# Performance work log

Measured on AMD Instinct MI355X. Metric: run time of the kernel, lower is better.

## Reference

```python
import jax, jax.numpy as jnp
import numpy as np
import math

B, T, D, H, K = 4, 2048, 1024, 16, 64

def setup_inputs() -> dict:
    key = jax.random.key(0)
    ks = jax.random.split(key, 6)
    scale = 1.0 / math.sqrt(D)  # keep logits in a sane range (torch code uses raw randn params)
    X = jax.random.normal(ks[0], (B, T, D), dtype=jnp.float32)
    Wq = jax.random.normal(ks[1], (H, D, K), dtype=jnp.float32) * scale
    Wk = jax.random.normal(ks[2], (H, D, K), dtype=jnp.float32) * scale
    Wv = jax.random.normal(ks[3], (H, D, K), dtype=jnp.float32) * scale
    Wo = jax.random.normal(ks[4], (H * K, H * K), dtype=jnp.float32) * (1.0 / math.sqrt(H * K))
    bo = jnp.zeros((H * K,), dtype=jnp.float32)
    return {"X": X, "Wq": Wq, "Wk": Wk, "Wv": Wv, "Wo": Wo, "bo": bo}

def reference(X, Wq, Wk, Wv, Wo, bo):
    # per-head projections: [B,H,T,K]
    q = jnp.einsum('btc,nck->bntk', X, Wq)
    k = jnp.einsum('btc,nck->bntk', X, Wk)
    v = jnp.einsum('btc,nck->bntk', X, Wv)
    # full score matrix [B,H,T,T] with causal mask (query t attends to s <= t)
    scores = jnp.einsum('bntk,bnsk->bnts', q, k) / math.sqrt(K)
    causal = jnp.tril(jnp.ones((T, T), dtype=bool))
    scores = jnp.where(causal[None, None], scores, jnp.finfo(scores.dtype).min)
    attn = jax.nn.softmax(scores, axis=-1)
    out = jnp.einsum('bnts,bnsk->bntk', attn, v)  # [B,H,T,K]
    # concat heads along feature dim (head-major ordering, matches torch.cat over heads)
    out = jnp.transpose(out, (0, 2, 1, 3)).reshape(B, T, H * K)
    # output projection (torch nn.Linear: x @ W.T + b)
    return out @ Wo.T + bo
```

## Files before the change

### kernel.cpp

```cpp
#include <hip/hip_runtime.h>
#include <hip/hip_bf16.h>
#include <math.h>

#define B_SZ 4
#define T_SZ 2048
#define D_SZ 1024
#define H_SZ 16
#define K_SZ 64

typedef __attribute__((ext_vector_type(8))) short bf8_t;
typedef __attribute__((ext_vector_type(4))) float f4_t;

__device__ __forceinline__ ushort f2bf(float f) {
    union { float f; unsigned u; } v; v.f = f;
    return (ushort)((v.u + 0x7fffu + ((v.u >> 16) & 1u)) >> 16);
}

__device__ __forceinline__ void gld_lds16(const ushort* g, ushort* l) {
    __builtin_amdgcn_global_load_lds(
        (const __attribute__((address_space(1))) void*)g,
        (__attribute__((address_space(3))) void*)l, 16, 0, 0);
}

__global__ __launch_bounds__(256) void convert_bf16_kernel(
    const float* __restrict__ src, ushort* __restrict__ dst)
{
    const size_t i = ((size_t)blockIdx.x * 256 + threadIdx.x) * 8;
    float4 a = *(const float4*)(src + i);
    float4 b = *(const float4*)(src + i + 4);
    ushort o[8] = {f2bf(a.x), f2bf(a.y), f2bf(a.z), f2bf(a.w),
                   f2bf(b.x), f2bf(b.y), f2bf(b.z), f2bf(b.w)};
    *(uint4*)(dst + i) = *(const uint4*)o;
}

__global__ __launch_bounds__(256) void transpose_w_kernel(
    const float* __restrict__ Wq, const float* __restrict__ Wk,
    const float* __restrict__ Wv, ushort* __restrict__ WT)
{
    __shared__ __align__(16) float tile[64][68];
    const int tid = threadIdx.x;
    const int d0  = blockIdx.x * 64;
    const int g   = blockIdx.y;
    const int sel = g >> 4, h = g & 15;
    const float* W = (sel == 0 ? Wq : (sel == 1 ? Wk : Wv)) + (size_t)h * D_SZ * K_SZ;

    {
        const int r = tid >> 2, ks = (tid & 3) * 16;
        const float4* src = (const float4*)(W + (size_t)(d0 + r) * 64 + ks);
        float4* dst = (float4*)&tile[r][ks];
        dst[0] = src[0]; dst[1] = src[1]; dst[2] = src[2]; dst[3] = src[3];
    }
    __syncthreads();
    {
        const int k = tid >> 2, ds = (tid & 3) * 16;
        ushort o[16];
        #pragma unroll
        for (int i = 0; i < 16; ++i) o[i] = f2bf(tile[ds + i][k]);
        uint4* dst = (uint4*)&WT[(size_t)(sel * 1024 + h * 64 + k) * 1024 + d0 + ds];
        dst[0] = ((const uint4*)o)[0];
        dst[1] = ((const uint4*)o)[1];
    }
}

__device__ __forceinline__ void gemm_bt_tile(
    const ushort* __restrict__ A, const ushort* __restrict__ Bt,
    int Kdim, int m0, int n0, ushort* As, ushort* Bs, f4_t acc[4][4])
{
    const int tid  = threadIdx.x;
    const int lane = tid & 63, wv = tid >> 6;
    const int l16  = lane & 15, quad = lane >> 4;
    const int wm   = (wv >> 1) * 64, wn = (wv & 1) * 64;
    const int sw   = (l16 >> 1) & 3;

    const int ra0 = tid >> 2,         qa0 = (tid & 3) ^ ((ra0 >> 1) & 3);
    const int ra1 = (tid + 256) >> 2, qa1 = (tid & 3) ^ ((ra1 >> 1) & 3);
    ushort* ldsA0 = As + (size_t)(wv * 64) * 8;
    ushort* ldsA1 = As + (size_t)(wv * 64 + 256) * 8;
    ushort* ldsB0 = Bs + (size_t)(wv * 64) * 8;
    ushort* ldsB1 = Bs + (size_t)(wv * 64 + 256) * 8;
    const ushort* gA0 = A  + (size_t)(m0 + ra0) * Kdim + qa0 * 8;
    const ushort* gA1 = A  + (size_t)(m0 + ra1) * Kdim + qa1 * 8;
    const ushort* gB0 = Bt + (size_t)(n0 + ra0) * Kdim + qa0 * 8;
    const ushort* gB1 = Bt + (size_t)(n0 + ra1) * Kdim + qa1 * 8;

    for (int k0 = 0; k0 < Kdim; k0 += 32) {
        __syncthreads();
        gld_lds16(gA0 + k0, ldsA0);
        gld_lds16(gA1 + k0, ldsA1);
        gld_lds16(gB0 + k0, ldsB0);
        gld_lds16(gB1 + k0, ldsB1);
        __syncthreads();

        bf8_t a[4], b[4];
        #pragma unroll
        for (int mt = 0; mt < 4; ++mt)
            a[mt] = *(const bf8_t*)&As[(wm + mt * 16 + l16) * 32 + ((quad ^ sw) * 8)];
        #pragma unroll
        for (int nt = 0; nt < 4; ++nt)
            b[nt] = *(const bf8_t*)&Bs[(wn + nt * 16 + l16) * 32 + ((quad ^ sw) * 8)];
        #pragma unroll
        for (int mt = 0; mt < 4; ++mt)
            #pragma unroll
            for (int nt = 0; nt < 4; ++nt)
                acc[mt][nt] = __builtin_amdgcn_mfma_f32_16x16x32_bf16(
                    a[mt], b[nt], acc[mt][nt], 0, 0, 0);
    }
}

__global__ __launch_bounds__(256) void gemm_qkv_kernel(
    const ushort* __restrict__ Xb, const ushort* __restrict__ WT,
    ushort* __restrict__ Qo, ushort* __restrict__ Ko, ushort* __restrict__ Vo)
{
    __shared__ __align__(16) ushort As[128 * 32];
    __shared__ __align__(16) ushort Bs[128 * 32];
    const int n0 = blockIdx.x * 128, m0 = blockIdx.y * 128;

    f4_t acc[4][4];
    #pragma unroll
    for (int i = 0; i < 4; ++i)
        #pragma unroll
        for (int j = 0; j < 4; ++j) acc[i][j] = (f4_t){0.f, 0.f, 0.f, 0.f};

    gemm_bt_tile(Xb, WT, 1024, m0, n0, As, Bs, acc);

    const int tid = threadIdx.x;
    const int lane = tid & 63, wv = tid >> 6;
    const int l16 = lane & 15, quad = lane >> 4;
    const int wm = (wv >> 1) * 64, wn = (wv & 1) * 64;
    const int sel = n0 >> 10;
    ushort* Out = (sel == 0 ? Qo : (sel == 1 ? Ko : Vo));
    const float osc = (sel == 0) ? 0.125f : 1.0f;

    #pragma unroll
    for (int nt = 0; nt < 4; ++nt) {
        const int col = n0 + wn + nt * 16 + l16;
        const int h = (col >> 6) & 15, kk = col & 63;
        #pragma unroll
        for (int mt = 0; mt < 4; ++mt) {
            #pragma unroll
            for (int r = 0; r < 4; ++r) {
                const int row = m0 + wm + mt * 16 + quad * 4 + r;
                const int bb = row >> 11, t = row & 2047;
                Out[((size_t)(bb * 16 + h) * 2048 + t) * 64 + kk] =
                    f2bf(acc[mt][nt][r] * osc);
            }
        }
    }
}

__global__ __launch_bounds__(256) void gemm_out_kernel(
    const ushort* __restrict__ Yb, const ushort* __restrict__ WoB,
    const float* __restrict__ bo, float* __restrict__ Out)
{
    __shared__ __align__(16) ushort As[128 * 32];
    __shared__ __align__(16) ushort Bs[128 * 32];
    const int n0 = blockIdx.x * 128, m0 = blockIdx.y * 128;

    f4_t acc[4][4];
    #pragma unroll
    for (int i = 0; i < 4; ++i)
        #pragma unroll
        for (int j = 0; j < 4; ++j) acc[i][j] = (f4_t){0.f, 0.f, 0.f, 0.f};

    gemm_bt_tile(Yb, WoB, 1024, m0, n0, As, Bs, acc);

    const int tid = threadIdx.x;
    const int lane = tid & 63, wv = tid >> 6;
    const int l16 = lane & 15, quad = lane >> 4;
    const int wm = (wv >> 1) * 64, wn = (wv & 1) * 64;

    #pragma unroll
    for (int nt = 0; nt < 4; ++nt) {
        const int col = n0 + wn + nt * 16 + l16;
        const float bias = bo[col];
        #pragma unroll
        for (int mt = 0; mt < 4; ++mt) {
            #pragma unroll
            for (int r = 0; r < 4; ++r) {
                const int row = m0 + wm + mt * 16 + quad * 4 + r;
                Out[(size_t)row * 1024 + col] = acc[mt][nt][r] + bias;
            }
        }
    }
}

__global__ __launch_bounds__(256) void transpose_v_kernel(
    const ushort* __restrict__ V, ushort* __restrict__ Vt)
{
    __shared__ __align__(16) ushort tile[64 * 74];
    const int tid = threadIdx.x;
    const int t0  = blockIdx.x * 64;
    const int bh  = blockIdx.y;

    {
        const int t = tid >> 2, ks = (tid & 3) * 16;
        const ushort* src = V + ((size_t)bh * T_SZ + t0 + t) * K_SZ + ks;
        uint4 a = *(const uint4*)src;
        uint4 b = *(const uint4*)(src + 8);
        uint* dst = (uint*)&tile[t * 74 + ks];
        dst[0] = a.x; dst[1] = a.y; dst[2] = a.z; dst[3] = a.w;
        dst[4] = b.x; dst[5] = b.y; dst[6] = b.z; dst[7] = b.w;
    }
    __syncthreads();
    {
        const int l = tid & 63, w = tid >> 6;
        #pragma unroll
        for (int kk = 0; kk < 16; ++kk) {
            const int k = w * 16 + kk;
            Vt[((size_t)bh * K_SZ + k) * T_SZ + t0 + l] = tile[l * 74 + k];
        }
    }
}

__global__ __launch_bounds__(256) void attn_mfma_kernel(
    const ushort* __restrict__ Qg, const ushort* __restrict__ Kg,
    const ushort* __restrict__ Vtg, ushort* __restrict__ Y)
{
    __shared__ __align__(16) ushort Ks[2][64 * 64];
    __shared__ __align__(16) ushort Vs[2][64 * 64];
    __shared__ __align__(16) ushort Pl[4][32 * 72];

    const int tid  = threadIdx.x;
    const int w    = tid >> 6;
    const int lane = tid & 63;
    const int l16  = lane & 15;
    const int quad = lane >> 4;
    const int qi = 15 - blockIdx.x;
    const int bh = blockIdx.y;
    const int bb = bh >> 4, h = bh & 15;

    const int Q0   = qi * 128;
    const int trow = Q0 + w * 32;

    bf8_t qa[2][2];
    #pragma unroll
    for (int mt = 0; mt < 2; ++mt) {
        const ushort* qp = Qg + ((size_t)bh * T_SZ + trow + mt * 16 + l16) * K_SZ + quad * 8;
        qa[mt][0] = *(const bf8_t*)qp;
        qa[mt][1] = *(const bf8_t*)(qp + 32);
    }

    f4_t O[2][4];
    #pragma unroll
    for (int mt = 0; mt < 2; ++mt)
        #pragma unroll
        for (int dt = 0; dt < 4; ++dt) O[mt][dt] = (f4_t){0.f, 0.f, 0.f, 0.f};
    float lp[2][4];
    #pragma unroll
    for (int mt = 0; mt < 2; ++mt)
        #pragma unroll
        for (int r = 0; r < 4; ++r) lp[mt][r] = 0.f;

    ushort* myP = Pl[w];
    const int sw_r = ((l16 >> 2) & 3) << 4;
    const int g_ln = (lane & 7) ^ (lane >> 3);
    const int rr_ln = lane >> 3;

    const ushort* Kbh = Kg  + (size_t)bh * T_SZ * K_SZ;
    const ushort* Vbh = Vtg + (size_t)bh * K_SZ * T_SZ;

    const int n_it = 2 * qi + 2;

    #pragma unroll
    for (int j = 0; j < 2; ++j) {
        const int r8 = (j * 4 + w) * 8 + rr_ln;
        gld_lds16(Kbh + (size_t)r8 * K_SZ + g_ln * 8, &Ks[0][(j * 4 + w) * 512]);
        gld_lds16(Vbh + (size_t)r8 * T_SZ + g_ln * 8, &Vs[0][(j * 4 + w) * 512]);
    }

    int cur = 0;
    for (int it = 0; it < n_it; ++it) {
        const int s0 = it * 64;

        __syncthreads();
        if (it + 1 < n_it) {
            const int sn = s0 + 64, nb = cur ^ 1;
            #pragma unroll
            for (int j = 0; j < 2; ++j) {
                const int r8 = (j * 4 + w) * 8 + rr_ln;
                gld_lds16(Kbh + (size_t)(sn + r8) * K_SZ + g_ln * 8,
                          &Ks[nb][(j * 4 + w) * 512]);
                gld_lds16(Vbh + (size_t)r8 * T_SZ + sn + g_ln * 8,
                          &Vs[nb][(j * 4 + w) * 512]);
            }
        }

        if (s0 < trow + 32) {
            const ushort* Kc = Ks[cur];
            const ushort* Vc = Vs[cur];

            bf8_t kb[4][2], vb[4][2];
            #pragma unroll
            for (int nt = 0; nt < 4; ++nt) {
                const int sr = nt * 16 + l16;
                kb[nt][0] = *(const bf8_t*)&Kc[sr * 64 + ((quad ^ (sr & 7)) * 8)];
                kb[nt][1] = *(const bf8_t*)&Kc[sr * 64 + (((quad + 4) ^ (sr & 7)) * 8)];
                vb[nt][0] = *(const bf8_t*)&Vc[sr * 64 + ((quad ^ (sr & 7)) * 8)];
                vb[nt][1] = *(const bf8_t*)&Vc[sr * 64 + (((quad + 4) ^ (sr & 7)) * 8)];
            }

            f4_t S[2][4];
            #pragma unroll
            for (int mt = 0; mt < 2; ++mt)
                #pragma unroll
                for (int nt = 0; nt < 4; ++nt) S[mt][nt] = (f4_t){0.f, 0.f, 0.f, 0.f};
            #pragma unroll
            for (int mt = 0; mt < 2; ++mt)
                #pragma unroll
                for (int nt = 0; nt < 4; ++nt) {
                    S[mt][nt] = __builtin_amdgcn_mfma_f32_16x16x32_bf16(
                        qa[mt][0], kb[nt][0], S[mt][nt], 0, 0, 0);
                    S[mt][nt] = __builtin_amdgcn_mfma_f32_16x16x32_bf16(
                        qa[mt][1], kb[nt][1], S[mt][nt], 0, 0, 0);
                }

            const bool diag = (s0 + 64 > trow);

            #pragma unroll
            for (int mt = 0; mt < 2; ++mt) {
                float p[4][4];
                #pragma unroll
                for (int nt = 0; nt < 4; ++nt) {
                    const int sg = s0 + nt * 16 + l16;
                    #pragma unroll
                    for (int r = 0; r < 4; ++r) {
                        float x = S[mt][nt][r];
                        if (diag && sg > trow + mt * 16 + quad * 4 + r) x = -1e30f;
                        p[nt][r] = __expf(x);
                        lp[mt][r] += p[nt][r];
                    }
                }
                #pragma unroll
                for (int nt = 0; nt < 4; ++nt) {
                    const int colp = (nt * 16 + l16) ^ (quad << 4);
                    #pragma unroll
                    for (int r = 0; r < 4; ++r)
                        myP[(mt * 16 + quad * 4 + r) * 72 + colp] = f2bf(p[nt][r]);
                }
            }
            asm volatile("" ::: "memory");
            bf8_t pa[2][2];
            #pragma unroll
            for (int mt = 0; mt < 2; ++mt) {
                const ushort* pr = &myP[(mt * 16 + l16) * 72];
                pa[mt][0] = *(const bf8_t*)(pr + ((quad * 8) ^ sw_r));
                pa[mt][1] = *(const bf8_t*)(pr + ((32 + quad * 8) ^ sw_r));
            }

            #pragma unroll
            for (int dt = 0; dt < 4; ++dt)
                #pragma unroll
                for (int mt = 0; mt < 2; ++mt) {
                    O[mt][dt] = __builtin_amdgcn_mfma_f32_16x16x32_bf16(
                        pa[mt][0], vb[dt][0], O[mt][dt], 0, 0, 0);
                    O[mt][dt] = __builtin_amdgcn_mfma_f32_16x16x32_bf16(
                        pa[mt][1], vb[dt][1], O[mt][dt], 0, 0, 0);
                }
        }
        cur ^= 1;
    }

    #pragma unroll
    for (int mt = 0; mt < 2; ++mt) {
        float inv[4];
        #pragma unroll
        for (int r = 0; r < 4; ++r) {
            float s = lp[mt][r];
            #pragma unroll
            for (int off = 1; off < 16; off <<= 1)
                s += __shfl_xor(s, off);
            inv[r] = 1.f / s;
        }
        #pragma unroll
        for (int dt = 0; dt < 4; ++dt) {
            const int col = h * 64 + dt * 16 + l16;
            #pragma unroll
            for (int r = 0; r < 4; ++r) {
                const int tg = trow + mt * 16 + quad * 4 + r;
                Y[((size_t)(bb * T_SZ + tg)) * (H_SZ * K_SZ) + col] =
                    f2bf(O[mt][dt][r] * inv[r]);
            }
        }
    }
}

extern "C" void kernel_launch(void* const* d_in, const int* in_sizes, int n_in,
                              void* d_out, int out_size, void* d_ws, size_t ws_size,
                              hipStream_t stream) {
    const float* X  = (const float*)d_in[0];
    const float* Wq = (const float*)d_in[1];
    const float* Wk = (const float*)d_in[2];
    const float* Wv = (const float*)d_in[3];
    const float* Wo = (const float*)d_in[4];
    const float* bo = (const float*)d_in[5];
    float* out = (float*)d_out;

    const size_t NE = (size_t)B_SZ * H_SZ * T_SZ * K_SZ;
    ushort* Qb   = (ushort*)d_ws;
    ushort* Kb   = Qb + NE;
    ushort* Vb   = Kb + NE;
    ushort* Vtb  = Vb + NE;
    ushort* Yb   = Vtb + NE;
    ushort* Xb   = Yb + NE;
    ushort* WT   = Xb + NE;
    ushort* WoB  = WT + (size_t)3072 * 1024;

    convert_bf16_kernel<<<dim3(4096), 256, 0, stream>>>(X, Xb);
    convert_bf16_kernel<<<dim3(512), 256, 0, stream>>>(Wo, WoB);
    transpose_w_kernel<<<dim3(16, 48), 256, 0, stream>>>(Wq, Wk, Wv, WT);
    gemm_qkv_kernel<<<dim3(24, 64), 256, 0, stream>>>(Xb, WT, Qb, Kb, Vb);
    transpose_v_kernel<<<dim3(32, 64), 256, 0, stream>>>(Vb, Vtb);
    attn_mfma_kernel<<<dim3(16, 64), 256, 0, stream>>>(Qb, Kb, Vtb, Yb);
    gemm_out_kernel<<<dim3(8, 64), 256, 0, stream>>>(Yb, WoB, bo, out);
}
```

Before: 339.6 us.

## Fuse V transpose into QKV GEMM, enlarge attention blocks, use exp2 softmax

The QKV GEMM epilogue now writes V directly in transposed layout, which removes the separate transpose kernel and its extra round trip through global memory. The attention kernel moves to 512-thread blocks covering 256 query rows, so each K/V tile loaded into LDS is shared by twice as many rows. Q is pre-scaled by log2(e)/sqrt(K) so the softmax can use exp2f, and masking zeroes the probability after exponentiation. Probabilities and Q/K outputs are packed into pairs with a hardware bf16 conversion. Larger blocks may reduce occupancy, and the causal workload is split into fewer, coarser pieces.

New measurement: 439.6 us. 29.4% more time.

```diff
diff --git a/kernel.cpp b/kernel.cpp
--- a/kernel.cpp
+++ b/kernel.cpp
@@ -11,9 +11,17 @@
 typedef __attribute__((ext_vector_type(8))) short bf8_t;
 typedef __attribute__((ext_vector_type(4))) float f4_t;
 
+#define QSCALE 0.18033688011112042f
+
 __device__ __forceinline__ ushort f2bf(float f) {
     union { float f; unsigned u; } v; v.f = f;
     return (ushort)((v.u + 0x7fffu + ((v.u >> 16) & 1u)) >> 16);
+}
+
+__device__ __forceinline__ uint pack2bf(float a, float b) {
+    union { __hip_bfloat162 h; uint u; } v;
+    v.h = __float22bfloat162_rn(make_float2(a, b));
+    return v.u;
 }
 
 __device__ __forceinline__ void gld_lds16(const ushort* g, ushort* l) {
@@ -109,7 +117,7 @@
 
 __global__ __launch_bounds__(256) void gemm_qkv_kernel(
     const ushort* __restrict__ Xb, const ushort* __restrict__ WT,
-    ushort* __restrict__ Qo, ushort* __restrict__ Ko, ushort* __restrict__ Vo)
+    ushort* __restrict__ Qo, ushort* __restrict__ Ko, ushort* __restrict__ Vt)
 {
     __shared__ __align__(16) ushort As[128 * 32];
     __shared__ __align__(16) ushort Bs[128 * 32];
@@ -128,21 +136,40 @@
     const int l16 = lane & 15, quad = lane >> 4;
     const int wm = (wv >> 1) * 64, wn = (wv & 1) * 64;
     const int sel = n0 >> 10;
-    ushort* Out = (sel == 0 ? Qo : (sel == 1 ? Ko : Vo));
-    const float osc = (sel == 0) ? 0.125f : 1.0f;
-
-    #pragma unroll
-    for (int nt = 0; nt < 4; ++nt) {
-        const int col = n0 + wn + nt * 16 + l16;
-        const int h = (col >> 6) & 15, kk = col & 63;
-        #pragma unroll
-        for (int mt = 0; mt < 4; ++mt) {
-            #pragma unroll
-            for (int r = 0; r < 4; ++r) {
-                const int row = m0 + wm + mt * 16 + quad * 4 + r;
-                const int bb = row >> 11, t = row & 2047;
-                Out[((size_t)(bb * 16 + h) * 2048 + t) * 64 + kk] =
-                    f2bf(acc[mt][nt][r] * osc);
+
+    if (sel < 2) {
+        ushort* Out = (sel == 0) ? Qo : Ko;
+        const float osc = (sel == 0) ? QSCALE : 1.0f;
+        #pragma unroll
+        for (int nt = 0; nt < 4; ++nt) {
+            const int col = n0 + wn + nt * 16 + l16;
+            const int h = (col >> 6) & 15, kk = col & 63;
+            #pragma unroll
+            for (int mt = 0; mt < 4; ++mt) {
+                const int row0 = m0 + wm + mt * 16 + quad * 4;
+                const int bb = row0 >> 11, t = row0 & 2047;
+                uint u01 = pack2bf(acc[mt][nt][0] * osc, acc[mt][nt][1] * osc);
+                uint u23 = pack2bf(acc[mt][nt][2] * osc, acc[mt][nt][3] * osc);
+                ushort* dst = &Out[((size_t)(bb * 16 + h) * 2048 + t) * 64 + kk];
+                dst[0]       = (ushort)u01;
+                dst[64]      = (ushort)(u01 >> 16);
+                dst[128]     = (ushort)u23;
+                dst[192]     = (ushort)(u23 >> 16);
+            }
+        }
+    } else {
+        #pragma unroll
+        for (int nt = 0; nt < 4; ++nt) {
+            const int col = n0 + wn + nt * 16 + l16;
+            const int h = (col >> 6) & 15, kk = col & 63;
+            #pragma unroll
+            for (int mt = 0; mt < 4; ++mt) {
+                const int row0 = m0 + wm + mt * 16 + quad * 4;
+                const int bb = row0 >> 11, t = row0 & 2047;
+                uint2 pk;
+                pk.x = pack2bf(acc[mt][nt][0], acc[mt][nt][1]);
+                pk.y = pack2bf(acc[mt][nt][2], acc[mt][nt][3]);
+                *(uint2*)&Vt[((size_t)((bb * 16 + h) * 64 + kk)) * 2048 + t] = pk;
             }
         }
     }
@@ -184,52 +211,24 @@
     }
 }
 
-__global__ __launch_bounds__(256) void transpose_v_kernel(
-    const ushort* __restrict__ V, ushort* __restrict__ Vt)
-{
-    __shared__ __align__(16) ushort tile[64 * 74];
-    const int tid = threadIdx.x;
-    const int t0  = blockIdx.x * 64;
-    const int bh  = blockIdx.y;
-
-    {
-        const int t = tid >> 2, ks = (tid & 3) * 16;
-        const ushort* src = V + ((size_t)bh * T_SZ + t0 + t) * K_SZ + ks;
-        uint4 a = *(const uint4*)src;
-        uint4 b = *(const uint4*)(src + 8);
-        uint* dst = (uint*)&tile[t * 74 + ks];
-        dst[0] = a.x; dst[1] = a.y; dst[2] = a.z; dst[3] = a.w;
-        dst[4] = b.x; dst[5] = b.y; dst[6] = b.z; dst[7] = b.w;
-    }
-    __syncthreads();
-    {
-        const int l = tid & 63, w = tid >> 6;
-        #pragma unroll
-        for (int kk = 0; kk < 16; ++kk) {
-            const int k = w * 16 + kk;
-            Vt[((size_t)bh * K_SZ + k) * T_SZ + t0 + l] = tile[l * 74 + k];
-        }
-    }
-}
-
-__global__ __launch_bounds__(256) void attn_mfma_kernel(
+__global__ __launch_bounds__(512, 4) void attn_mfma_kernel(
     const ushort* __restrict__ Qg, const ushort* __restrict__ Kg,
     const ushort* __restrict__ Vtg, ushort* __restrict__ Y)
 {
     __shared__ __align__(16) ushort Ks[2][64 * 64];
     __shared__ __align__(16) ushort Vs[2][64 * 64];
-    __shared__ __align__(16) ushort Pl[4][32 * 72];
+    __shared__ __align__(16) ushort Pl[8][32 * 72];
 
     const int tid  = threadIdx.x;
     const int w    = tid >> 6;
     const int lane = tid & 63;
     const int l16  = lane & 15;
     const int quad = lane >> 4;
-    const int qi = 15 - blockIdx.x;
+    const int qi = 7 - blockIdx.x;
     const int bh = blockIdx.y;
     const int bb = bh >> 4, h = bh & 15;
 
-    const int Q0   = qi * 128;
+    const int Q0   = qi * 256;
     const int trow = Q0 + w * 32;
 
     bf8_t qa[2][2];
@@ -253,20 +252,16 @@
 
     ushort* myP = Pl[w];
     const int sw_r = ((l16 >> 2) & 3) << 4;
-    const int g_ln = (lane & 7) ^ (lane >> 3);
-    const int rr_ln = lane >> 3;
+    const int g_ln  = (lane & 7) ^ (lane >> 3);
+    const int srow  = w * 8 + (lane >> 3);
 
     const ushort* Kbh = Kg  + (size_t)bh * T_SZ * K_SZ;
     const ushort* Vbh = Vtg + (size_t)bh * K_SZ * T_SZ;
 
-    const int n_it = 2 * qi + 2;
-
-    #pragma unroll
-    for (int j = 0; j < 2; ++j) {
-        const int r8 = (j * 4 + w) * 8 + rr_ln;
-        gld_lds16(Kbh + (size_t)r8 * K_SZ + g_ln * 8, &Ks[0][(j * 4 + w) * 512]);
-        gld_lds16(Vbh + (size_t)r8 * T_SZ + g_ln * 8, &Vs[0][(j * 4 + w) * 512]);
-    }
+    const int n_it = 4 * qi + 4;
+
+    gld_lds16(Kbh + (size_t)srow * K_SZ + g_ln * 8, &Ks[0][w * 512]);
+    gld_lds16(Vbh + (size_t)srow * T_SZ + g_ln * 8, &Vs[0][w * 512]);
 
     int cur = 0;
     for (int it = 0; it < n_it; ++it) {
@@ -275,14 +270,8 @@
         __syncthreads();
         if (it + 1 < n_it) {
             const int sn = s0 + 64, nb = cur ^ 1;
-            #pragma unroll
-            for (int j = 0; j < 2; ++j) {
-                const int r8 = (j * 4 + w) * 8 + rr_ln;
-                gld_lds16(Kbh + (size_t)(sn + r8) * K_SZ + g_ln * 8,
-                          &Ks[nb][(j * 4 + w) * 512]);
-                gld_lds16(Vbh + (size_t)r8 * T_SZ + sn + g_ln * 8,
-                          &Vs[nb][(j * 4 + w) * 512]);
-            }
+            gld_lds16(Kbh + (size_t)(sn + srow) * K_SZ + g_ln * 8, &Ks[nb][w * 512]);
+            gld_lds16(Vbh + (size_t)srow * T_SZ + sn + g_ln * 8,  &Vs[nb][w * 512]);
         }
 
         if (s0 < trow + 32) {
@@ -324,18 +313,22 @@
                     const int sg = s0 + nt * 16 + l16;
                     #pragma unroll
                     for (int r = 0; r < 4; ++r) {
-                        float x = S[mt][nt][r];
-                        if (diag && sg > trow + mt * 16 + quad * 4 + r) x = -1e30f;
-                        p[nt][r] = __expf(x);
-                        lp[mt][r] += p[nt][r];
+                        float pv = exp2f(S[mt][nt][r]);
+                        if (diag && sg > trow + mt * 16 + quad * 4 + r) pv = 0.f;
+                        p[nt][r] = pv;
+                        lp[mt][r] += pv;
                     }
                 }
                 #pragma unroll
                 for (int nt = 0; nt < 4; ++nt) {
                     const int colp = (nt * 16 + l16) ^ (quad << 4);
-                    #pragma unroll
-                    for (int r = 0; r < 4; ++r)
-                        myP[(mt * 16 + quad * 4 + r) * 72 + colp] = f2bf(p[nt][r]);
+                    uint u01 = pack2bf(p[nt][0], p[nt][1]);
+                    uint u23 = pack2bf(p[nt][2], p[nt][3]);
+                    ushort* pw = &myP[(mt * 16 + quad * 4) * 72 + colp];
+                    pw[0]       = (ushort)u01;
+                    pw[72]      = (ushort)(u01 >> 16);
+                    pw[144]     = (ushort)u23;
+                    pw[216]     = (ushort)(u23 >> 16);
                 }
             }
             asm volatile("" ::: "memory");
@@ -398,8 +391,7 @@
     const size_t NE = (size_t)B_SZ * H_SZ * T_SZ * K_SZ;
     ushort* Qb   = (ushort*)d_ws;
     ushort* Kb   = Qb + NE;
-    ushort* Vb   = Kb + NE;
-    ushort* Vtb  = Vb + NE;
+    ushort* Vtb  = Kb + NE;
     ushort* Yb   = Vtb + NE;
     ushort* Xb   = Yb + NE;
     ushort* WT   = Xb + NE;
@@ -408,8 +400,7 @@
     convert_bf16_kernel<<<dim3(4096), 256, 0, stream>>>(X, Xb);
     convert_bf16_kernel<<<dim3(512), 256, 0, stream>>>(Wo, WoB);
     transpose_w_kernel<<<dim3(16, 48), 256, 0, stream>>>(Wq, Wk, Wv, WT);
-    gemm_qkv_kernel<<<dim3(24, 64), 256, 0, stream>>>(Xb, WT, Qb, Kb, Vb);
-    transpose_v_kernel<<<dim3(32, 64), 256, 0, stream>>>(Vb, Vtb);
-    attn_mfma_kernel<<<dim3(16, 64), 256, 0, stream>>>(Qb, Kb, Vtb, Yb);
+    gemm_qkv_kernel<<<dim3(24, 64), 256, 0, stream>>>(Xb, WT, Qb, Kb, Vtb);
+    attn_mfma_kernel<<<dim3(8, 64), 512, 0, stream>>>(Qb, Kb, Vtb, Yb);
     gemm_out_kernel<<<dim3(8, 64), 256, 0, stream>>>(Yb, WoB, bo, out);
 }
```
